# Performance work log

Hardware: AMD Instinct MI355X
Metric: run time of the kernel (lower is better)

## Reference

```python
import jax, jax.numpy as jnp
import numpy as np

ALPHA = 0.25
GAMMA = 2.0
EPS = 1e-8
COST_CLASS = 1.0
COST_BBOX = 1.0
COST_GIOU = 1.0


def segment_cw_to_t1t2(x):
    # x: [..., 2] = (center, width) -> (t1, t2)
    c, w = x[..., 0], x[..., 1]
    return jnp.stack([c - 0.5 * w, c + 0.5 * w], axis=-1)


def segment_iou(a, b):
    # a: [N, 2], b: [M, 2] -> pairwise IoU [N, M]
    lt = jnp.maximum(a[:, None, 0], b[None, :, 0])
    rb = jnp.minimum(a[:, None, 1], b[None, :, 1])
    inter = jnp.clip(rb - lt, 0.0)
    union = (a[:, 1] - a[:, 0])[:, None] + (b[:, 1] - b[:, 0])[None, :] - inter
    return inter / jnp.maximum(union, EPS)


def setup_inputs() -> dict:
    key = jax.random.key(0)
    k1, k2, k3, k4, k5, k6 = jax.random.split(key, 6)
    bs, Q, n_cls, M = 16, 2000, 80, 1024
    pred_logits = jax.random.normal(k1, (bs, Q, n_cls), dtype=jnp.float32)
    # boxes layout: [t1, t2, center, width] with t1<=t2 and width>0 (valid segments)
    p_t = jnp.sort(jax.random.uniform(k2, (bs, Q, 2), dtype=jnp.float32), axis=-1)
    p_cw = jax.random.uniform(k3, (bs, Q, 2), dtype=jnp.float32) * jnp.array([1.0, 0.5]) + jnp.array([0.0, 0.05])
    pred_boxes = jnp.concatenate([p_t, p_cw], axis=-1)
    t_t = jnp.sort(jax.random.uniform(k4, (M, 2), dtype=jnp.float32), axis=-1)
    t_cw = jax.random.uniform(k5, (M, 2), dtype=jnp.float32) * jnp.array([1.0, 0.5]) + jnp.array([0.0, 0.05])
    tgt_bbox = jnp.concatenate([t_t, t_cw], axis=-1)
    tgt_ids = jax.random.randint(k6, (M,), 0, n_cls, dtype=jnp.int64 if jax.config.jax_enable_x64 else jnp.int32)
    return {"pred_logits": pred_logits, "pred_boxes": pred_boxes,
            "tgt_ids": tgt_ids, "tgt_bbox": tgt_bbox}


def reference(pred_logits, pred_boxes, tgt_ids, tgt_bbox):
    bs, Q, _ = pred_logits.shape
    out_prob = jax.nn.softmax(pred_logits.reshape(bs * Q, -1), axis=-1)  # [bs*Q, n_cls]
    out_bbox = pred_boxes.reshape(bs * Q, 4)
    # focal-style classification cost
    neg_cost = (1.0 - ALPHA) * out_prob ** GAMMA * (-jnp.log1p(-out_prob + EPS))
    pos_cost = ALPHA * (1.0 - out_prob) ** GAMMA * (-jnp.log(out_prob + EPS))
    cost_class = pos_cost[:, tgt_ids] - neg_cost[:, tgt_ids]  # [bs*Q, M]
    # L1 box cost (cdist p=1)
    cost_bbox = jnp.sum(jnp.abs(out_bbox[:, None, :] - tgt_bbox[None, :, :]), axis=-1)
    # GIoU-style cost: average of IoU over (c,w)->t1t2 segments and raw t1t2 segments
    cost_giou = -(segment_iou(segment_cw_to_t1t2(out_bbox[:, 2:]), segment_cw_to_t1t2(tgt_bbox[:, 2:]))
                  + segment_iou(out_bbox[:, :2], tgt_bbox[:, :2])) / 2.0
    C = COST_BBOX * cost_bbox + COST_CLASS * cost_class + COST_GIOU * cost_giou
    return C.reshape(bs, Q, -1)
```

## Files before the change

kernel.cpp:

```cpp
#include <hip/hip_runtime.h>
#include <math.h>

#define ALPHA 0.25f
#define EPS 1e-8f

typedef float f4v __attribute__((ext_vector_type(4)));

constexpr int NCLS = 80;
constexpr int Mn = 1024;
constexpr int RPB = 8;

__global__ __launch_bounds__(256, 5) void matcher_kernel(
    const float* __restrict__ logits,
    const float* __restrict__ pboxes,
    const int*   __restrict__ tids,
    const float* __restrict__ tboxes,
    float* __restrict__ out)
{
    __shared__ float cls[RPB][NCLS];

    const int tid  = threadIdx.x;
    const int row0 = blockIdx.x * RPB;

    const int j0 = tid * 4;
    float t1[4], t2[4], tc[4], th[4], wr[4];
    int id[4];
    #pragma unroll
    for (int k = 0; k < 4; ++k) {
        float4 b = *(const float4*)(tboxes + (size_t)(j0 + k) * 4);
        t1[k] = b.x;
        t2[k] = b.y;
        tc[k] = b.z;
        th[k] = 0.5f * b.w;
        wr[k] = b.y - b.x;
        id[k] = tids[j0 + k];
    }

    if (tid < 160) {
        ((float4*)&cls[0][0])[tid] =
            ((const float4*)(logits + (size_t)row0 * NCLS))[tid];
    }
    __syncthreads();

    {
        const int r = tid >> 5;
        const int c = tid & 31;
        const int c2 = (c < 16) ? c + 64 : c;
        float l0 = cls[r][c];
        float l1 = cls[r][c + 32];
        float l2 = cls[r][c2];
        float e0 = __expf(l0);
        float e1 = __expf(l1);
        float e2 = (c < 16) ? __expf(l2) : 0.0f;
        float s = e0 + e1 + e2;
        #pragma unroll
        for (int off = 16; off; off >>= 1) s += __shfl_xor(s, off);
        float inv_s = __builtin_amdgcn_rcpf(s);
        float p0 = e0 * inv_s, p1 = e1 * inv_s, p2 = e2 * inv_s;
        float o0 = 1.0f - p0, o1 = 1.0f - p1, o2 = 1.0f - p2;
        float cc0 = ALPHA * o0 * o0 * (-__logf(p0 + EPS))
                  - (1.0f - ALPHA) * p0 * p0 * (-__logf(o0 + EPS));
        float cc1 = ALPHA * o1 * o1 * (-__logf(p1 + EPS))
                  - (1.0f - ALPHA) * p1 * p1 * (-__logf(o1 + EPS));
        float cc2 = ALPHA * o2 * o2 * (-__logf(p2 + EPS))
                  - (1.0f - ALPHA) * p2 * p2 * (-__logf(o2 + EPS));
        cls[r][c]      = cc0;
        cls[r][c + 32] = cc1;
        if (c < 16) cls[r][c + 64] = cc2;
    }
    __syncthreads();

    #pragma unroll 2
    for (int r = 0; r < RPB; ++r) {
        const float4 pb = *(const float4*)(pboxes + (size_t)(row0 + r) * 4);
        const float pwr = pb.y - pb.x;
        const float phw = 0.5f * pb.w;

        f4v res;
        #pragma unroll
        for (int k = 0; k < 4; ++k) {
            float d1 = pb.x - t1[k];
            float d2 = pb.y - t2[k];
            float dc = pb.z - tc[k];
            float dw = phw - th[k];
            float ab = fabsf(d1) + fabsf(d2);
            float db = ab + fmaf(fabsf(dw), 2.0f, fabsf(dc));
            float P1 = fmaf(2.0f, th[k], pb.w);
            float m1 = fmaxf(fabsf(dc), fabsf(dw));
            float A1 = fmaxf(fmaf(-2.0f, m1, P1), 0.0f);
            float D1 = fmaxf(fmaf(2.0f, P1, -A1), 2.0f * EPS);
            float P2 = pwr + wr[k];
            float A2 = fmaxf(P2 - ab, 0.0f);
            float D2 = fmaxf(fmaf(2.0f, P2, -A2), 2.0f * EPS);
            float num = A1 * D2 + A2 * D1;
            float inv = __builtin_amdgcn_rcpf(D1 * D2);
            res[k] = fmaf(num * inv, -0.5f, db + cls[r][id[k]]);
        }
        *(f4v*)(out + (size_t)(row0 + r) * Mn + j0) = res;
    }
}

extern "C" void kernel_launch(void* const* d_in, const int* in_sizes, int n_in,
                              void* d_out, int out_size, void* d_ws, size_t ws_size,
                              hipStream_t stream) {
    const float* logits = (const float*)d_in[0];
    const float* pboxes = (const float*)d_in[1];
    const int*   tids   = (const int*)d_in[2];
    const float* tboxes = (const float*)d_in[3];
    float* out = (float*)d_out;

    const int total_rows = in_sizes[0] / NCLS;
    const int nblocks = total_rows / RPB;
    matcher_kernel<<<nblocks, 256, 0, stream>>>(logits, pboxes, tids, tboxes, out);
}
```

Measured before the change: 36.29 us.

## Process 16 rows per block and compute softmax directly from global logits

Doubles the rows per block from 8 to 16 so the per-thread target box setup is amortized over more output rows, and raises the occupancy hint in launch bounds. The logits are now read straight from global memory into registers by 16 threads per row, with the softmax and focal cost computed in one phase. This removes one shared-memory staging pass and one barrier. The main loop also preloads the gathered class costs before the box math and unrolls further. The stricter launch bounds may cap registers and cause spills, and half as many blocks means less parallelism across the GPU.

```diff
diff --git a/kernel.cpp b/kernel.cpp
--- a/kernel.cpp
+++ b/kernel.cpp
@@ -8,9 +8,9 @@
 
 constexpr int NCLS = 80;
 constexpr int Mn = 1024;
-constexpr int RPB = 8;
+constexpr int RPB = 16;
 
-__global__ __launch_bounds__(256, 5) void matcher_kernel(
+__global__ __launch_bounds__(256, 8) void matcher_kernel(
     const float* __restrict__ logits,
     const float* __restrict__ pboxes,
     const int*   __restrict__ tids,
@@ -36,45 +36,43 @@
         id[k] = tids[j0 + k];
     }
 
-    if (tid < 160) {
-        ((float4*)&cls[0][0])[tid] =
-            ((const float4*)(logits + (size_t)row0 * NCLS))[tid];
+    {
+        const int r = tid >> 4;
+        const int c = tid & 15;
+        const float* lrow = logits + (size_t)(row0 + r) * NCLS + c;
+        float e0 = __expf(lrow[0]);
+        float e1 = __expf(lrow[16]);
+        float e2 = __expf(lrow[32]);
+        float e3 = __expf(lrow[48]);
+        float e4 = __expf(lrow[64]);
+        float s = ((e0 + e1) + (e2 + e3)) + e4;
+        s += __shfl_xor(s, 1);
+        s += __shfl_xor(s, 2);
+        s += __shfl_xor(s, 4);
+        s += __shfl_xor(s, 8);
+        float inv_s = __builtin_amdgcn_rcpf(s);
+        float* crow = &cls[r][c];
+        float e[5] = {e0, e1, e2, e3, e4};
+        #pragma unroll
+        for (int k = 0; k < 5; ++k) {
+            float p = e[k] * inv_s;
+            float o = 1.0f - p;
+            crow[16 * k] = ALPHA * o * o * (-__logf(p + EPS))
+                         - (1.0f - ALPHA) * p * p * (-__logf(o + EPS));
+        }
     }
     __syncthreads();
 
-    {
-        const int r = tid >> 5;
-        const int c = tid & 31;
-        const int c2 = (c < 16) ? c + 64 : c;
-        float l0 = cls[r][c];
-        float l1 = cls[r][c + 32];
-        float l2 = cls[r][c2];
-        float e0 = __expf(l0);
-        float e1 = __expf(l1);
-        float e2 = (c < 16) ? __expf(l2) : 0.0f;
-        float s = e0 + e1 + e2;
-        #pragma unroll
-        for (int off = 16; off; off >>= 1) s += __shfl_xor(s, off);
-        float inv_s = __builtin_amdgcn_rcpf(s);
-        float p0 = e0 * inv_s, p1 = e1 * inv_s, p2 = e2 * inv_s;
-        float o0 = 1.0f - p0, o1 = 1.0f - p1, o2 = 1.0f - p2;
-        float cc0 = ALPHA * o0 * o0 * (-__logf(p0 + EPS))
-                  - (1.0f - ALPHA) * p0 * p0 * (-__logf(o0 + EPS));
-        float cc1 = ALPHA * o1 * o1 * (-__logf(p1 + EPS))
-                  - (1.0f - ALPHA) * p1 * p1 * (-__logf(o1 + EPS));
-        float cc2 = ALPHA * o2 * o2 * (-__logf(p2 + EPS))
-                  - (1.0f - ALPHA) * p2 * p2 * (-__logf(o2 + EPS));
-        cls[r][c]      = cc0;
-        cls[r][c + 32] = cc1;
-        if (c < 16) cls[r][c + 64] = cc2;
-    }
-    __syncthreads();
-
-    #pragma unroll 2
+    float* outp = out + (size_t)row0 * Mn + j0;
+    #pragma unroll 4
     for (int r = 0; r < RPB; ++r) {
         const float4 pb = *(const float4*)(pboxes + (size_t)(row0 + r) * 4);
         const float pwr = pb.y - pb.x;
         const float phw = 0.5f * pb.w;
+
+        float ccv[4];
+        #pragma unroll
+        for (int k = 0; k < 4; ++k) ccv[k] = cls[r][id[k]];
 
         f4v res;
         #pragma unroll
@@ -94,9 +92,9 @@
             float D2 = fmaxf(fmaf(2.0f, P2, -A2), 2.0f * EPS);
             float num = A1 * D2 + A2 * D1;
             float inv = __builtin_amdgcn_rcpf(D1 * D2);
-            res[k] = fmaf(num * inv, -0.5f, db + cls[r][id[k]]);
+            res[k] = fmaf(num * inv, -0.5f, db + ccv[k]);
         }
-        *(f4v*)(out + (size_t)(row0 + r) * Mn + j0) = res;
+        *(f4v*)(outp + (size_t)r * Mn) = res;
     }
 }
 
```

Result: no change. 36.30 us (+0.0%).
